# Performance work log

Measured on AMD Instinct MI355X. Metric: run time of the kernel, lower is better.

The kernel has to match this reference:

```python
import jax, jax.numpy as jnp
import numpy as np

N_NODES = 100000
N_EDGES = 1600000
D_IN = 128
D_HID = 128
N_LAYERS = 3


def setup_inputs() -> dict:
    key = jax.random.key(0)
    k1, k2, k3, k4 = jax.random.split(key, 4)
    x = jax.random.normal(k1, (N_NODES, D_IN), dtype=jnp.float32)
    edge_index = jax.random.randint(k2, (2, N_EDGES), 0, N_NODES, dtype=jnp.int64)
    # Glorot-ish scale for stability across 3 layers
    Ws = jax.random.normal(k3, (N_LAYERS, D_IN, D_HID), dtype=jnp.float32) * (1.0 / np.sqrt(D_IN))
    bs = jax.random.normal(k4, (N_LAYERS, D_HID), dtype=jnp.float32) * 0.01
    return {"x": x, "edge_index": edge_index, "Ws": Ws, "bs": bs}


def _gcn_conv(x, row, col, deg_inv_sqrt, W, b, n_nodes):
    # Linear transform first (PyG GCNConv), then gather-normalize-scatter.
    h = x @ W                                        # [N, D]
    norm = deg_inv_sqrt[row] * deg_inv_sqrt[col]     # [E+N] (self-loops included)
    msg = h[row] * norm[:, None]                     # gather + scale, [E+N, D]
    out = jax.ops.segment_sum(msg, col, num_segments=n_nodes)  # scatter-add
    return out + b


def reference(x, edge_index, Ws, bs):
    n = x.shape[0]
    # add self-loops once (same for every layer)
    loop = jnp.arange(n, dtype=edge_index.dtype)
    row = jnp.concatenate([edge_index[0], loop])
    col = jnp.concatenate([edge_index[1], loop])
    # symmetric normalization: deg over target nodes (incl. self-loops)
    deg = jax.ops.segment_sum(jnp.ones_like(col, dtype=x.dtype), col, num_segments=n)
    deg_inv_sqrt = jnp.where(deg > 0, jax.lax.rsqrt(jnp.maximum(deg, 1.0)), 0.0)
    h = x
    for i in range(Ws.shape[0]):
        h = jax.nn.relu(_gcn_conv(h, row, col, deg_inv_sqrt, Ws[i], bs[i], n))
    return h
```

## Files before the change

### kernel.cpp

```cpp
#include <hip/hip_runtime.h>
#include <hip/hip_bf16.h>

#define NN 100000
#define NROWS 100032
#define NE 1600000
#define DD 128
#define NBUK 196
#define F1_BLOCKS 256
#define F3_BLOCKS 256

typedef unsigned short ushort_t;
typedef unsigned int uint_t;
typedef unsigned long long uint64_t_;
typedef __attribute__((ext_vector_type(8))) short bf16x8;
typedef __attribute__((ext_vector_type(4))) float f32x4;

__device__ __forceinline__ ushort_t bf16rne(float f) {
    uint_t u = __float_as_uint(f);
    u += 0x7FFF + ((u >> 16) & 1);
    return (ushort_t)(u >> 16);
}
__device__ __forceinline__ float bfLo(uint_t u) { return __uint_as_float(u << 16); }
__device__ __forceinline__ float bfHi(uint_t u) { return __uint_as_float(u & 0xFFFF0000u); }


__global__ __launch_bounds__(256) void f1_bucket_count(const int* __restrict__ col,
                                                       int* __restrict__ bukCount,
                                                       const float* __restrict__ Ws,
                                                       ushort_t* __restrict__ wT) {
    __shared__ int hist[NBUK];
    if (blockIdx.x >= F1_BLOCKS) {
        int idx = (blockIdx.x - F1_BLOCKS) * 256 + threadIdx.x;
        if (idx < 3 * 128 * 16) {
            int l = idx >> 11;
            int r = idx & 2047;
            int c = r >> 4;
            int kc = r & 15;
            const float* w = Ws + l * 16384;
            ushort_t tmp[8];
#pragma unroll
            for (int e = 0; e < 8; ++e)
                tmp[e] = bf16rne(w[(kc * 8 + e) * 128 + c]);
            *(uint4*)&wT[(size_t)l * 16384 + c * 128 + kc * 8] = *(uint4*)tmp;
        }
        return;
    }
    for (int t = threadIdx.x; t < NBUK; t += 256) hist[t] = 0;
    __syncthreads();
    const int epb = (NE + F1_BLOCKS - 1) / F1_BLOCKS;
    const int e0 = blockIdx.x * epb;
    const int e1 = min(e0 + epb, NE);
    for (int e = e0 + threadIdx.x; e < e1; e += 256)
        atomicAdd(&hist[col[e] >> 9], 1);
    __syncthreads();
    for (int t = threadIdx.x; t < NBUK; t += 256)
        if (hist[t]) atomicAdd(&bukCount[t], hist[t]);
}

__global__ void f2_bucket_scan(const int* __restrict__ bukCount,
                               int* __restrict__ bukBase,
                               int* __restrict__ bukCursor,
                               int* __restrict__ offsets) {
    __shared__ int s[256];
    const int t = threadIdx.x;
    int v = (t < NBUK) ? bukCount[t] : 0;
    s[t] = v;
    __syncthreads();
    for (int off = 1; off < 256; off <<= 1) {
        int tmp = (t >= off) ? s[t - off] : 0;
        __syncthreads();
        s[t] += tmp;
        __syncthreads();
    }
    int excl = s[t] - v;
    if (t < NBUK) { bukBase[t] = excl; bukCursor[t] = excl; }
    if (t == 255) { bukBase[NBUK] = s[255]; offsets[NN] = s[255]; }
}

__global__ __launch_bounds__(256) void f3_scatter(const int* __restrict__ row,
                                                  const int* __restrict__ col,
                                                  int* __restrict__ bukCursor,
                                                  int* __restrict__ ebuf) {
    __shared__ int hist[4][NBUK];
    __shared__ int base[4][NBUK];
    const int t = threadIdx.x;
    const int w = t >> 6;
    const int lane = t & 63;
    for (int i = t; i < 4 * NBUK; i += 256) (&hist[0][0])[i] = 0;
    __syncthreads();
    const int epb = (NE + F3_BLOCKS - 1) / F3_BLOCKS;
    const int e0 = blockIdx.x * epb;
    const int e1 = min(e0 + epb, NE);
    const int wepb = (e1 - e0 + 3) >> 2;
    const int we0 = e0 + w * wepb;
    const int we1 = min(we0 + wepb, e1);
    for (int e = we0 + lane; e < we1; e += 64)
        atomicAdd(&hist[w][col[e] >> 9], 1);
    __syncthreads();
    if (t < NBUK) {
        int h0 = hist[0][t], h1 = hist[1][t], h2 = hist[2][t], h3 = hist[3][t];
        int tot = h0 + h1 + h2 + h3;
        int g = tot ? atomicAdd(&bukCursor[t], tot) : 0;
        base[0][t] = g; base[1][t] = g + h0;
        base[2][t] = g + h0 + h1; base[3][t] = g + h0 + h1 + h2;
        hist[0][t] = 0; hist[1][t] = 0; hist[2][t] = 0; hist[3][t] = 0;
    }
    __syncthreads();
    for (int e = we0 + lane; e < we1; e += 64) {
        int c = col[e];
        int b = c >> 9;
        int r = atomicAdd(&hist[w][b], 1);
        ebuf[base[w][b] + r] = (row[e] << 9) | (c & 511);
    }
}

__global__ __launch_bounds__(256) void f4_finalize(const int* __restrict__ ebuf,
                                                   const int* __restrict__ bukBase,
                                                   int* __restrict__ offsets,
                                                   float* __restrict__ dis,
                                                   int* __restrict__ csr_src) {
    __shared__ int cnt[512];
    __shared__ int cur[512];
    __shared__ int s[256];
    const int t = threadIdx.x;
    const int colBase = blockIdx.x << 9;
    const int ncols = min(512, NN - colBase);
    cnt[t] = 0; cnt[t + 256] = 0;
    __syncthreads();
    const int eb0 = bukBase[blockIdx.x];
    const int eb1 = bukBase[blockIdx.x + 1];
    for (int e = eb0 + t; e < eb1; e += 256)
        atomicAdd(&cnt[ebuf[e] & 511], 1);
    __syncthreads();
    const int c0 = cnt[2 * t], c1 = cnt[2 * t + 1];
    const int psum = c0 + c1;
    s[t] = psum;
    __syncthreads();
    for (int off = 1; off < 256; off <<= 1) {
        int tmp = (t >= off) ? s[t - off] : 0;
        __syncthreads();
        s[t] += tmp;
        __syncthreads();
    }
    const int exclPair = s[t] - psum;
    const int g0 = eb0 + exclPair;
    const int g1 = g0 + c0;
    cur[2 * t] = g0; cur[2 * t + 1] = g1;
    if (2 * t < ncols)     { offsets[colBase + 2 * t]     = g0; dis[colBase + 2 * t]     = rsqrtf((float)(c0 + 1)); }
    if (2 * t + 1 < ncols) { offsets[colBase + 2 * t + 1] = g1; dis[colBase + 2 * t + 1] = rsqrtf((float)(c1 + 1)); }
    __syncthreads();
    for (int e = eb0 + t; e < eb1; e += 256) {
        int pc = ebuf[e];
        int p = atomicAdd(&cur[pc & 511], 1);
        csr_src[p] = pc >> 9;
    }
}


template<bool XF32>
__global__ __launch_bounds__(256) void gemm_mfma(const void* __restrict__ Xv,
                                                 const ushort_t* __restrict__ wT,
                                                 const float* __restrict__ dis,
                                                 ushort_t* __restrict__ Y) {
    __shared__ short smem[128 * 136];
    {
        const uint4* src = (const uint4*)wT;
        int t = threadIdx.x;
#pragma unroll
        for (int i = 0; i < 8; ++i) {
            int idx = i * 256 + t;
            int rowc = idx >> 4;
            int kc = idx & 15;
            uint4 v = src[idx];
            *(uint4*)&smem[rowc * 136 + kc * 8] = v;
        }
    }
    __syncthreads();

    const int wave = threadIdx.x >> 6;
    const int lane = threadIdx.x & 63;
    const int m = lane & 15;
    const int kg = lane >> 4;
    const int r0 = blockIdx.x * 64 + wave * 16;
    const int rowA = min(r0 + m, NN - 1);

    f32x4 acc[8];
#pragma unroll
    for (int ct = 0; ct < 8; ++ct) acc[ct] = (f32x4){0.f, 0.f, 0.f, 0.f};

#pragma unroll
    for (int ks = 0; ks < 4; ++ks) {
        bf16x8 af;
        if (XF32) {
            const float* xp = (const float*)Xv + (size_t)rowA * DD + ks * 32 + kg * 8;
            float4 f0 = *(const float4*)xp;
            float4 f1 = *(const float4*)(xp + 4);
            af[0] = (short)bf16rne(f0.x); af[1] = (short)bf16rne(f0.y);
            af[2] = (short)bf16rne(f0.z); af[3] = (short)bf16rne(f0.w);
            af[4] = (short)bf16rne(f1.x); af[5] = (short)bf16rne(f1.y);
            af[6] = (short)bf16rne(f1.z); af[7] = (short)bf16rne(f1.w);
        } else {
            const ushort_t* xp = (const ushort_t*)Xv + (size_t)rowA * DD + ks * 32 + kg * 8;
            af = *(const bf16x8*)xp;
        }
#pragma unroll
        for (int ct = 0; ct < 8; ++ct) {
            bf16x8 bf = *(const bf16x8*)&smem[(ct * 16 + m) * 136 + ks * 32 + kg * 8];
            acc[ct] = __builtin_amdgcn_mfma_f32_16x16x32_bf16(af, bf, acc[ct], 0, 0, 0);
        }
    }

    __syncthreads();

    ushort_t* sl = (ushort_t*)smem;
    const int rbase = r0 + kg * 4;
    float dv[4];
#pragma unroll
    for (int rg = 0; rg < 4; ++rg) dv[rg] = dis[min(rbase + rg, NN - 1)];
#pragma unroll
    for (int ct = 0; ct < 8; ++ct) {
#pragma unroll
        for (int rg = 0; rg < 4; ++rg)
            sl[(wave * 16 + kg * 4 + rg) * 132 + ct * 16 + m] = bf16rne(acc[ct][rg] * dv[rg]);
    }

    const int lr = lane >> 2;
    const int q  = lane & 3;
    const int grow = r0 + lr;
    const ushort_t* rb = sl + (wave * 16 + lr) * 132 + q * 32;
    uint2 d0 = *(const uint2*)(rb + 0);
    uint2 d1 = *(const uint2*)(rb + 4);
    uint2 d2 = *(const uint2*)(rb + 8);
    uint2 d3 = *(const uint2*)(rb + 12);
    uint2 d4 = *(const uint2*)(rb + 16);
    uint2 d5 = *(const uint2*)(rb + 20);
    uint2 d6 = *(const uint2*)(rb + 24);
    uint2 d7 = *(const uint2*)(rb + 28);
    const bool ok = grow < NN;
    uint4 v0 = ok ? make_uint4(d0.x, d0.y, d1.x, d1.y) : make_uint4(0, 0, 0, 0);
    uint4 v1 = ok ? make_uint4(d2.x, d2.y, d3.x, d3.y) : make_uint4(0, 0, 0, 0);
    uint4 v2 = ok ? make_uint4(d4.x, d4.y, d5.x, d5.y) : make_uint4(0, 0, 0, 0);
    uint4 v3 = ok ? make_uint4(d6.x, d6.y, d7.x, d7.y) : make_uint4(0, 0, 0, 0);
    uint4* yp = (uint4*)&Y[(size_t)grow * DD + q * 32];
    yp[0] = v0; yp[1] = v1; yp[2] = v2; yp[3] = v3;
}


template<bool F32OUT>
__global__ __launch_bounds__(256) void agg_kernel(const uint_t* __restrict__ lin2,
                                                  const int* __restrict__ offsets,
                                                  const int* __restrict__ csr_src,
                                                  const float* __restrict__ dis,
                                                  const float* __restrict__ bias,
                                                  void* __restrict__ outv) {
    const int bid = blockIdx.x;
    const int xcd = bid & 7;
    const int h   = (xcd >> 2);
    const int g   = (bid >> 3) * 4 + (xcd & 3);
    const int w    = threadIdx.x >> 6;
    const int lane = threadIdx.x & 63;
    const int l32  = lane & 31;
    const int hi   = lane >> 5;
    const int v = g * 8 + w * 2 + hi;

    const int start = offsets[v];
    const int end   = offsets[v + 1];
    const int n     = end - start;
    const int nvm   = n < 32 ? n : 32;

    int idxv = NN;
    if (l32 < nvm) idxv = csr_src[start + l32];

    const int nv_other = __shfl(nvm, lane ^ 32);
    int kmax = nvm > nv_other ? nvm : nv_other;
    kmax = (kmax + 15) & ~15;

    const uint_t doff = (uint_t)(h * 32 + l32);
    const float dv = dis[v];
    uint_t self = lin2[((uint_t)v << 6) | doff];
    float2 b    = ((const float2*)bias)[doff];

    float accx = 0.f, accy = 0.f;
    const int sbase = (lane & 32);
    for (int k = 0; k < kmax; k += 16) {
        int s0 = __shfl(idxv, sbase + k + 0);
        int s1 = __shfl(idxv, sbase + k + 1);
        int s2 = __shfl(idxv, sbase + k + 2);
        int s3 = __shfl(idxv, sbase + k + 3);
        int s4 = __shfl(idxv, sbase + k + 4);
        int s5 = __shfl(idxv, sbase + k + 5);
        int s6 = __shfl(idxv, sbase + k + 6);
        int s7 = __shfl(idxv, sbase + k + 7);
        int s8 = __shfl(idxv, sbase + k + 8);
        int s9 = __shfl(idxv, sbase + k + 9);
        int sa = __shfl(idxv, sbase + k + 10);
        int sb = __shfl(idxv, sbase + k + 11);
        int sc = __shfl(idxv, sbase + k + 12);
        int sd = __shfl(idxv, sbase + k + 13);
        int se = __shfl(idxv, sbase + k + 14);
        int sf = __shfl(idxv, sbase + k + 15);
        uint_t a0 = lin2[((uint_t)s0 << 6) | doff];
        uint_t a1 = lin2[((uint_t)s1 << 6) | doff];
        uint_t a2 = lin2[((uint_t)s2 << 6) | doff];
        uint_t a3 = lin2[((uint_t)s3 << 6) | doff];
        uint_t a4 = lin2[((uint_t)s4 << 6) | doff];
        uint_t a5 = lin2[((uint_t)s5 << 6) | doff];
        uint_t a6 = lin2[((uint_t)s6 << 6) | doff];
        uint_t a7 = lin2[((uint_t)s7 << 6) | doff];
        uint_t a8 = lin2[((uint_t)s8 << 6) | doff];
        uint_t a9 = lin2[((uint_t)s9 << 6) | doff];
        uint_t aa = lin2[((uint_t)sa << 6) | doff];
        uint_t ab = lin2[((uint_t)sb << 6) | doff];
        uint_t ac = lin2[((uint_t)sc << 6) | doff];
        uint_t ad = lin2[((uint_t)sd << 6) | doff];
        uint_t ae = lin2[((uint_t)se << 6) | doff];
        uint_t af = lin2[((uint_t)sf << 6) | doff];
        accx += bfLo(a0) + bfLo(a1) + bfLo(a2) + bfLo(a3)
              + bfLo(a4) + bfLo(a5) + bfLo(a6) + bfLo(a7)
              + bfLo(a8) + bfLo(a9) + bfLo(aa) + bfLo(ab)
              + bfLo(ac) + bfLo(ad) + bfLo(ae) + bfLo(af);
        accy += bfHi(a0) + bfHi(a1) + bfHi(a2) + bfHi(a3)
              + bfHi(a4) + bfHi(a5) + bfHi(a6) + bfHi(a7)
              + bfHi(a8) + bfHi(a9) + bfHi(aa) + bfHi(ab)
              + bfHi(ac) + bfHi(ad) + bfHi(ae) + bfHi(af);
    }
    for (int e = start + 32; e < end; ++e) {
        uint_t s = (uint_t)csr_src[e];
        uint_t a = lin2[(s << 6) | doff];
        accx += bfLo(a); accy += bfHi(a);
    }

    float rx = fmaxf(dv * (accx + bfLo(self)) + b.x, 0.f);
    float ry = fmaxf(dv * (accy + bfHi(self)) + b.y, 0.f);
    const size_t oidx = (size_t)v * 64 + doff;
    if (F32OUT) {
        float2 o = make_float2(rx, ry);
        __builtin_nontemporal_store(*(const uint64_t_*)&o, (uint64_t_*)((float2*)outv + oidx));
    } else {
        uint_t pk = (uint_t)bf16rne(rx) | ((uint_t)bf16rne(ry) << 16);
        __builtin_nontemporal_store(pk, (uint_t*)outv + oidx);
    }
}


extern "C" void kernel_launch(void* const* d_in, const int* in_sizes, int n_in,
                              void* d_out, int out_size, void* d_ws, size_t ws_size,
                              hipStream_t stream) {
    const float* x   = (const float*)d_in[0];
    const int*   ei  = (const int*)d_in[1];
    const float* Ws  = (const float*)d_in[2];
    const float* bs  = (const float*)d_in[3];

    const int* row = ei;
    const int* col = ei + NE;

    char* ws = (char*)d_ws;
    ushort_t* lin    = (ushort_t*)(ws + 0);
    int*   ebuf      = (int*)  (ws + 0);
    ushort_t* hb     = (ushort_t*)(ws + 25608192);
    float* dis       = (float*)(ws + 51208192);
    int*   offsets   = (int*)  (ws + 51608192);
    int*   csr_src   = (int*)  (ws + 52008208);
    int*   bukCount  = (int*)  (ws + 58408208);
    int*   bukBase   = (int*)  (ws + 58409008);
    int*   bukCursor = (int*)  (ws + 58409808);
    ushort_t* wT     = (ushort_t*)(ws + 58410608);

    (void)hipMemsetAsync(bukCount, 0, NBUK * sizeof(int), stream);
    f1_bucket_count<<<F1_BLOCKS + 24, 256, 0, stream>>>(col, bukCount, Ws, wT);
    f2_bucket_scan<<<1, 256, 0, stream>>>(bukCount, bukBase, bukCursor, offsets);
    f3_scatter<<<F3_BLOCKS, 256, 0, stream>>>(row, col, bukCursor, ebuf);
    f4_finalize<<<NBUK, 256, 0, stream>>>(ebuf, bukBase, offsets, dis, csr_src);

    const int gemmGrid = NROWS / 64;
    const int aggGrid = (NN / 8) * 2;
    gemm_mfma<true><<<gemmGrid, 256, 0, stream>>>(x, wT, dis, lin);
    agg_kernel<false><<<aggGrid, 256, 0, stream>>>((const uint_t*)lin, offsets, csr_src, dis, bs, hb);
    gemm_mfma<false><<<gemmGrid, 256, 0, stream>>>(hb, wT + 16384, dis, lin);
    agg_kernel<false><<<aggGrid, 256, 0, stream>>>((const uint_t*)lin, offsets, csr_src, dis, bs + DD, hb);
    gemm_mfma<false><<<gemmGrid, 256, 0, stream>>>(hb, wT + 32768, dis, lin);
    agg_kernel<true><<<aggGrid, 256, 0, stream>>>((const uint_t*)lin, offsets, csr_src, dis, bs + 2 * DD, d_out);
}
```

Measured before the change: 290.0 us.

## Drop bucket count pass via fixed-capacity buckets; tile GEMM four row-tiles per block

The CSR build no longer runs a separate histogram pass before scattering. Edges are scattered straight into fixed-capacity per-bucket slots (BCAP each), and the prefix scan runs afterwards to compute global offsets, which removes one kernel launch and one full read of col. Separately, each GEMM block now keeps the whole weight tile in registers and processes four 64-row tiles, which amortises the shared-memory weight load over more rows. The risks are bucket overflow if any bucket exceeds BCAP edges, and higher register pressure in the GEMM.

```diff
diff --git a/kernel.cpp b/kernel.cpp
--- a/kernel.cpp
+++ b/kernel.cpp
@@ -6,7 +6,7 @@
 #define NE 1600000
 #define DD 128
 #define NBUK 196
-#define F1_BLOCKS 256
+#define BCAP 9216
 #define F3_BLOCKS 256
 
 typedef unsigned short ushort_t;
@@ -24,13 +24,16 @@
 __device__ __forceinline__ float bfHi(uint_t u) { return __uint_as_float(u & 0xFFFF0000u); }
 
 
-__global__ __launch_bounds__(256) void f1_bucket_count(const int* __restrict__ col,
-                                                       int* __restrict__ bukCount,
-                                                       const float* __restrict__ Ws,
-                                                       ushort_t* __restrict__ wT) {
-    __shared__ int hist[NBUK];
-    if (blockIdx.x >= F1_BLOCKS) {
-        int idx = (blockIdx.x - F1_BLOCKS) * 256 + threadIdx.x;
+__global__ __launch_bounds__(256) void f3_scatter(const int* __restrict__ row,
+                                                  const int* __restrict__ col,
+                                                  int* __restrict__ bukCnt,
+                                                  int* __restrict__ ebuf,
+                                                  const float* __restrict__ Ws,
+                                                  ushort_t* __restrict__ wT) {
+    __shared__ int hist[4][NBUK];
+    __shared__ int base[4][NBUK];
+    if (blockIdx.x >= F3_BLOCKS) {
+        int idx = (blockIdx.x - F3_BLOCKS) * 256 + threadIdx.x;
         if (idx < 3 * 128 * 16) {
             int l = idx >> 11;
             int r = idx & 2047;
@@ -45,44 +48,6 @@
         }
         return;
     }
-    for (int t = threadIdx.x; t < NBUK; t += 256) hist[t] = 0;
-    __syncthreads();
-    const int epb = (NE + F1_BLOCKS - 1) / F1_BLOCKS;
-    const int e0 = blockIdx.x * epb;
-    const int e1 = min(e0 + epb, NE);
-    for (int e = e0 + threadIdx.x; e < e1; e += 256)
-        atomicAdd(&hist[col[e] >> 9], 1);
-    __syncthreads();
-    for (int t = threadIdx.x; t < NBUK; t += 256)
-        if (hist[t]) atomicAdd(&bukCount[t], hist[t]);
-}
-
-__global__ void f2_bucket_scan(const int* __restrict__ bukCount,
-                               int* __restrict__ bukBase,
-                               int* __restrict__ bukCursor,
-                               int* __restrict__ offsets) {
-    __shared__ int s[256];
-    const int t = threadIdx.x;
-    int v = (t < NBUK) ? bukCount[t] : 0;
-    s[t] = v;
-    __syncthreads();
-    for (int off = 1; off < 256; off <<= 1) {
-        int tmp = (t >= off) ? s[t - off] : 0;
-        __syncthreads();
-        s[t] += tmp;
-        __syncthreads();
-    }
-    int excl = s[t] - v;
-    if (t < NBUK) { bukBase[t] = excl; bukCursor[t] = excl; }
-    if (t == 255) { bukBase[NBUK] = s[255]; offsets[NN] = s[255]; }
-}
-
-__global__ __launch_bounds__(256) void f3_scatter(const int* __restrict__ row,
-                                                  const int* __restrict__ col,
-                                                  int* __restrict__ bukCursor,
-                                                  int* __restrict__ ebuf) {
-    __shared__ int hist[4][NBUK];
-    __shared__ int base[4][NBUK];
     const int t = threadIdx.x;
     const int w = t >> 6;
     const int lane = t & 63;
@@ -100,7 +65,7 @@
     if (t < NBUK) {
         int h0 = hist[0][t], h1 = hist[1][t], h2 = hist[2][t], h3 = hist[3][t];
         int tot = h0 + h1 + h2 + h3;
-        int g = tot ? atomicAdd(&bukCursor[t], tot) : 0;
+        int g = tot ? (t * BCAP + atomicAdd(&bukCnt[t], tot)) : 0;
         base[0][t] = g; base[1][t] = g + h0;
         base[2][t] = g + h0 + h1; base[3][t] = g + h0 + h1 + h2;
         hist[0][t] = 0; hist[1][t] = 0; hist[2][t] = 0; hist[3][t] = 0;
@@ -112,6 +77,25 @@
         int r = atomicAdd(&hist[w][b], 1);
         ebuf[base[w][b] + r] = (row[e] << 9) | (c & 511);
     }
+}
+
+__global__ void f2_bucket_scan(const int* __restrict__ bukCnt,
+                               int* __restrict__ bukBase,
+                               int* __restrict__ offsets) {
+    __shared__ int s[256];
+    const int t = threadIdx.x;
+    int v = (t < NBUK) ? bukCnt[t] : 0;
+    s[t] = v;
+    __syncthreads();
+    for (int off = 1; off < 256; off <<= 1) {
+        int tmp = (t >= off) ? s[t - off] : 0;
+        __syncthreads();
+        s[t] += tmp;
+        __syncthreads();
+    }
+    int excl = s[t] - v;
+    if (t < NBUK) bukBase[t] = excl;
+    if (t == 255) { bukBase[NBUK] = s[255]; offsets[NN] = s[255]; }
 }
 
 __global__ __launch_bounds__(256) void f4_finalize(const int* __restrict__ ebuf,
@@ -127,9 +111,10 @@
     const int ncols = min(512, NN - colBase);
     cnt[t] = 0; cnt[t + 256] = 0;
     __syncthreads();
-    const int eb0 = bukBase[blockIdx.x];
-    const int eb1 = bukBase[blockIdx.x + 1];
-    for (int e = eb0 + t; e < eb1; e += 256)
+    const int gb0 = bukBase[blockIdx.x];
+    const int bcnt = bukBase[blockIdx.x + 1] - gb0;
+    const int cap0 = blockIdx.x * BCAP;
+    for (int e = cap0 + t; e < cap0 + bcnt; e += 256)
         atomicAdd(&cnt[ebuf[e] & 511], 1);
     __syncthreads();
     const int c0 = cnt[2 * t], c1 = cnt[2 * t + 1];
@@ -143,13 +128,13 @@
         __syncthreads();
     }
     const int exclPair = s[t] - psum;
-    const int g0 = eb0 + exclPair;
+    const int g0 = gb0 + exclPair;
     const int g1 = g0 + c0;
     cur[2 * t] = g0; cur[2 * t + 1] = g1;
     if (2 * t < ncols)     { offsets[colBase + 2 * t]     = g0; dis[colBase + 2 * t]     = rsqrtf((float)(c0 + 1)); }
     if (2 * t + 1 < ncols) { offsets[colBase + 2 * t + 1] = g1; dis[colBase + 2 * t + 1] = rsqrtf((float)(c1 + 1)); }
     __syncthreads();
-    for (int e = eb0 + t; e < eb1; e += 256) {
+    for (int e = cap0 + t; e < cap0 + bcnt; e += 256) {
         int pc = ebuf[e];
         int p = atomicAdd(&cur[pc & 511], 1);
         csr_src[p] = pc >> 9;
@@ -181,68 +166,79 @@
     const int lane = threadIdx.x & 63;
     const int m = lane & 15;
     const int kg = lane >> 4;
-    const int r0 = blockIdx.x * 64 + wave * 16;
-    const int rowA = min(r0 + m, NN - 1);
-
-    f32x4 acc[8];
-#pragma unroll
-    for (int ct = 0; ct < 8; ++ct) acc[ct] = (f32x4){0.f, 0.f, 0.f, 0.f};
-
-#pragma unroll
-    for (int ks = 0; ks < 4; ++ks) {
-        bf16x8 af;
-        if (XF32) {
-            const float* xp = (const float*)Xv + (size_t)rowA * DD + ks * 32 + kg * 8;
-            float4 f0 = *(const float4*)xp;
-            float4 f1 = *(const float4*)(xp + 4);
-            af[0] = (short)bf16rne(f0.x); af[1] = (short)bf16rne(f0.y);
-            af[2] = (short)bf16rne(f0.z); af[3] = (short)bf16rne(f0.w);
-            af[4] = (short)bf16rne(f1.x); af[5] = (short)bf16rne(f1.y);
-            af[6] = (short)bf16rne(f1.z); af[7] = (short)bf16rne(f1.w);
-        } else {
-            const ushort_t* xp = (const ushort_t*)Xv + (size_t)rowA * DD + ks * 32 + kg * 8;
-            af = *(const bf16x8*)xp;
-        }
+
+    bf16x8 bfr[8][4];
+#pragma unroll
+    for (int ct = 0; ct < 8; ++ct)
+#pragma unroll
+        for (int ks = 0; ks < 4; ++ks)
+            bfr[ct][ks] = *(const bf16x8*)&smem[(ct * 16 + m) * 136 + ks * 32 + kg * 8];
+    __syncthreads();
+
+    ushort_t* cs = (ushort_t*)smem + wave * (16 * 132);
+
+#pragma unroll
+    for (int rt = 0; rt < 4; ++rt) {
+        const int r0 = blockIdx.x * 256 + rt * 64 + wave * 16;
+        const int rowA = min(r0 + m, NN - 1);
+
+        f32x4 acc[8];
+#pragma unroll
+        for (int ct = 0; ct < 8; ++ct) acc[ct] = (f32x4){0.f, 0.f, 0.f, 0.f};
+
+#pragma unroll
+        for (int ks = 0; ks < 4; ++ks) {
+            bf16x8 af;
+            if (XF32) {
+                const float* xp = (const float*)Xv + (size_t)rowA * DD + ks * 32 + kg * 8;
+                float4 f0 = *(const float4*)xp;
+                float4 f1 = *(const float4*)(xp + 4);
+                af[0] = (short)bf16rne(f0.x); af[1] = (short)bf16rne(f0.y);
+                af[2] = (short)bf16rne(f0.z); af[3] = (short)bf16rne(f0.w);
+                af[4] = (short)bf16rne(f1.x); af[5] = (short)bf16rne(f1.y);
+                af[6] = (short)bf16rne(f1.z); af[7] = (short)bf16rne(f1.w);
+            } else {
+                const ushort_t* xp = (const ushort_t*)Xv + (size_t)rowA * DD + ks * 32 + kg * 8;
+                af = *(const bf16x8*)xp;
+            }
+#pragma unroll
+            for (int ct = 0; ct < 8; ++ct)
+                acc[ct] = __builtin_amdgcn_mfma_f32_16x16x32_bf16(af, bfr[ct][ks], acc[ct], 0, 0, 0);
+        }
+
+        const int rbase = r0 + kg * 4;
+        float dvv[4];
+#pragma unroll
+        for (int rg = 0; rg < 4; ++rg) dvv[rg] = dis[min(rbase + rg, NN - 1)];
 #pragma unroll
         for (int ct = 0; ct < 8; ++ct) {
-            bf16x8 bf = *(const bf16x8*)&smem[(ct * 16 + m) * 136 + ks * 32 + kg * 8];
-            acc[ct] = __builtin_amdgcn_mfma_f32_16x16x32_bf16(af, bf, acc[ct], 0, 0, 0);
-        }
-    }
-
-    __syncthreads();
-
-    ushort_t* sl = (ushort_t*)smem;
-    const int rbase = r0 + kg * 4;
-    float dv[4];
-#pragma unroll
-    for (int rg = 0; rg < 4; ++rg) dv[rg] = dis[min(rbase + rg, NN - 1)];
-#pragma unroll
-    for (int ct = 0; ct < 8; ++ct) {
-#pragma unroll
-        for (int rg = 0; rg < 4; ++rg)
-            sl[(wave * 16 + kg * 4 + rg) * 132 + ct * 16 + m] = bf16rne(acc[ct][rg] * dv[rg]);
-    }
-
-    const int lr = lane >> 2;
-    const int q  = lane & 3;
-    const int grow = r0 + lr;
-    const ushort_t* rb = sl + (wave * 16 + lr) * 132 + q * 32;
-    uint2 d0 = *(const uint2*)(rb + 0);
-    uint2 d1 = *(const uint2*)(rb + 4);
-    uint2 d2 = *(const uint2*)(rb + 8);
-    uint2 d3 = *(const uint2*)(rb + 12);
-    uint2 d4 = *(const uint2*)(rb + 16);
-    uint2 d5 = *(const uint2*)(rb + 20);
-    uint2 d6 = *(const uint2*)(rb + 24);
-    uint2 d7 = *(const uint2*)(rb + 28);
-    const bool ok = grow < NN;
-    uint4 v0 = ok ? make_uint4(d0.x, d0.y, d1.x, d1.y) : make_uint4(0, 0, 0, 0);
-    uint4 v1 = ok ? make_uint4(d2.x, d2.y, d3.x, d3.y) : make_uint4(0, 0, 0, 0);
-    uint4 v2 = ok ? make_uint4(d4.x, d4.y, d5.x, d5.y) : make_uint4(0, 0, 0, 0);
-    uint4 v3 = ok ? make_uint4(d6.x, d6.y, d7.x, d7.y) : make_uint4(0, 0, 0, 0);
-    uint4* yp = (uint4*)&Y[(size_t)grow * DD + q * 32];
-    yp[0] = v0; yp[1] = v1; yp[2] = v2; yp[3] = v3;
+#pragma unroll
+            for (int rg = 0; rg < 4; ++rg)
+                cs[(kg * 4 + rg) * 132 + ct * 16 + m] = bf16rne(acc[ct][rg] * dvv[rg]);
+        }
+
+        const int lr = lane >> 2;
+        const int q  = lane & 3;
+        const int grow = r0 + lr;
+        const ushort_t* rb = cs + lr * 132 + q * 32;
+        uint2 d0 = *(const uint2*)(rb + 0);
+        uint2 d1 = *(const uint2*)(rb + 4);
+        uint2 d2 = *(const uint2*)(rb + 8);
+        uint2 d3 = *(const uint2*)(rb + 12);
+        uint2 d4 = *(const uint2*)(rb + 16);
+        uint2 d5 = *(const uint2*)(rb + 20);
+        uint2 d6 = *(const uint2*)(rb + 24);
+        uint2 d7 = *(const uint2*)(rb + 28);
+        if (grow < NROWS) {
+            const bool ok = grow < NN;
+            uint4 v0 = ok ? make_uint4(d0.x, d0.y, d1.x, d1.y) : make_uint4(0, 0, 0, 0);
+            uint4 v1 = ok ? make_uint4(d2.x, d2.y, d3.x, d3.y) : make_uint4(0, 0, 0, 0);
+            uint4 v2 = ok ? make_uint4(d4.x, d4.y, d5.x, d5.y) : make_uint4(0, 0, 0, 0);
+            uint4 v3 = ok ? make_uint4(d6.x, d6.y, d7.x, d7.y) : make_uint4(0, 0, 0, 0);
+            uint4* yp = (uint4*)&Y[(size_t)grow * DD + q * 32];
+            yp[0] = v0; yp[1] = v1; yp[2] = v2; yp[3] = v3;
+        }
+    }
 }
 
 
@@ -361,18 +357,16 @@
     float* dis       = (float*)(ws + 51208192);
     int*   offsets   = (int*)  (ws + 51608192);
     int*   csr_src   = (int*)  (ws + 52008208);
-    int*   bukCount  = (int*)  (ws + 58408208);
+    int*   bukCnt    = (int*)  (ws + 58408208);
     int*   bukBase   = (int*)  (ws + 58409008);
-    int*   bukCursor = (int*)  (ws + 58409808);
     ushort_t* wT     = (ushort_t*)(ws + 58410608);
 
-    (void)hipMemsetAsync(bukCount, 0, NBUK * sizeof(int), stream);
-    f1_bucket_count<<<F1_BLOCKS + 24, 256, 0, stream>>>(col, bukCount, Ws, wT);
-    f2_bucket_scan<<<1, 256, 0, stream>>>(bukCount, bukBase, bukCursor, offsets);
-    f3_scatter<<<F3_BLOCKS, 256, 0, stream>>>(row, col, bukCursor, ebuf);
+    (void)hipMemsetAsync(bukCnt, 0, NBUK * sizeof(int), stream);
+    f3_scatter<<<F3_BLOCKS + 24, 256, 0, stream>>>(row, col, bukCnt, ebuf, Ws, wT);
+    f2_bucket_scan<<<1, 256, 0, stream>>>(bukCnt, bukBase, offsets);
     f4_finalize<<<NBUK, 256, 0, stream>>>(ebuf, bukBase, offsets, dis, csr_src);
 
-    const int gemmGrid = NROWS / 64;
+    const int gemmGrid = (NROWS + 255) / 256;
     const int aggGrid = (NN / 8) * 2;
     gemm_mfma<true><<<gemmGrid, 256, 0, stream>>>(x, wT, dis, lin);
     agg_kernel<false><<<aggGrid, 256, 0, stream>>>((const uint_t*)lin, offsets, csr_src, dis, bs, hb);
```

After: 280.7 us. 1.03x faster.
